# Kernel tuning notes

Measured on AMD Instinct MI355X. Metric: run time of the kernel, lower is better.

The kernel has to match this reference:

```python
import jax, jax.numpy as jnp
import numpy as np

# ---- static config (mirrors VectorQuantizer2.__init__) ----
V_PATCH = [1, 2, 3, 4, 6, 9, 13, 18, 24, 32]
SN = len(V_PATCH)
BETA = 0.25
QRESI = 0.5                      # Phi.resi_ratio = |quant_resi|
K_PHI = 4                        # share_quant_resi (PhiPartiallyShared)
TICKS = np.linspace(1.0 / 3 / K_PHI, 1.0 - 1.0 / 3 / K_PHI, K_PHI)  # K==4 branch
_A = -0.75                       # torch bicubic kernel coefficient


def _cubic(x):
    x = np.abs(x)
    return np.where(x <= 1.0, ((_A + 2.0) * x - (_A + 3.0)) * x * x + 1.0,
           np.where(x < 2.0, _A * (((x - 5.0) * x + 8.0) * x - 4.0), 0.0))


def _resize_mat(n_in, n_out, align_corners):
    # [n_out, n_in] separable torch-bicubic interpolation matrix (border-replicated)
    M = np.zeros((n_out, n_in), np.float32)
    for o in range(n_out):
        if align_corners:
            src = 0.0 if n_out == 1 else o * (n_in - 1) / (n_out - 1)
        else:
            src = (o + 0.5) * n_in / n_out - 0.5
        fl = int(np.floor(src)); t = src - fl
        for k in range(-1, 3):
            M[o, min(max(fl + k, 0), n_in - 1)] += float(_cubic(k - t))
    return jnp.asarray(M)


def _resize(x, hw, align_corners):
    # x: [B,C,H,W] -> [B,C,hw[0],hw[1]], bicubic, separable matmuls
    Mh = _resize_mat(x.shape[2], hw[0], align_corners)
    Mw = _resize_mat(x.shape[3], hw[1], align_corners)
    return jnp.einsum('oh,pw,bchw->bcop', Mh, Mw, x)


def _phi(h, w, b, r):
    # Phi: h*(1-r) + Conv3x3(h)*r
    y = jax.lax.conv_general_dilated(h, w, (1, 1), 'SAME',
                                     dimension_numbers=('NCHW', 'OIHW', 'NCHW'))
    y = y + b[None, :, None, None]
    return h * (1.0 - r) + y * r


def setup_inputs() -> dict:
    key = jax.random.key(0)
    k1, k2, k3 = jax.random.split(key, 3)
    B, C, H, W, V = 1024, 64, 32, 1, 4096
    f = jax.random.normal(k1, (B, C, H, W), jnp.float32)
    emb_weight = jax.random.normal(k2, (V, C), jnp.float32) * 0.02
    phi_w = jax.random.normal(k3, (K_PHI, C, C, 3, 3), jnp.float32) / np.sqrt(C * 9.0)
    phi_b = jnp.zeros((K_PHI, C), jnp.float32)
    return {"f_BChw": f, "emb_weight": emb_weight, "phi_w": phi_w, "phi_b": phi_b}


def reference(f_BChw, emb_weight, phi_w, phi_b):
    f = f_BChw.astype(jnp.float32)
    B, C, H, W = f.shape
    f_ng = jax.lax.stop_gradient(f)
    f_rest = f_ng
    f_hat = jnp.zeros_like(f_ng)
    e_ng = jax.lax.stop_gradient(emb_weight)
    e_sq = jnp.sum(e_ng * e_ng, axis=1)          # [V]
    loss = jnp.float32(0.0)
    levels = []
    for si, pn in enumerate(V_PATCH):
        ph, pw = pn, 1
        if si != SN - 1:
            rest = _resize(f_rest, (ph, pw), align_corners=True)
        else:
            rest = f                                  # last scale quantizes f itself
        rest_NC = jax.lax.stop_gradient(rest.transpose(0, 2, 3, 1).reshape(-1, C))
        d = jnp.sum(rest_NC * rest_NC, axis=1, keepdims=True) + e_sq \
            - 2.0 * (rest_NC @ e_ng.T)                # [N, V] squared distances
        idx = jnp.argmin(d, axis=1)                   # [N]
        h = emb_weight[idx.reshape(B, ph, pw)].transpose(0, 3, 1, 2)  # [B,C,ph,pw]
        if si != SN - 1:
            h = _resize(h, (H, W), align_corners=False)
        pi = int(np.argmin(np.abs(TICKS - si / (SN - 1))))
        h = _phi(h, phi_w[pi], phi_b[pi], QRESI)
        f_hat = f_hat + h
        f_rest = f_rest - h
        loss = loss + BETA * jnp.mean((jax.lax.stop_gradient(f_hat) - f) ** 2) \
                    + jnp.mean((f_hat - f_ng) ** 2)
        levels.append(f_hat)
    loss = loss / SN
    f_hat_st = jax.lax.stop_gradient(f_hat) - f_ng + f   # straight-through
    return f_hat_st, loss, jnp.stack(levels)
```

## Files before the change

kernel.cpp:

```cpp
#include <hip/hip_runtime.h>
#include <math.h>

#define BB 1024
#define CC 64
#define HH 32
#define VV 4096
#define NEL (BB*CC*HH)

#define RT 128

typedef __attribute__((ext_vector_type(4))) float f32x4;
typedef __attribute__((ext_vector_type(8))) short bf16x8;


__device__ double dev_cubic(double x){
#pragma clang fp contract(off)
  const double A = -0.75;
  x = fabs(x);
  if (x <= 1.0) return ((A + 2.0)*x - (A + 3.0))*x*x + 1.0;
  if (x < 2.0)  return A*(((x - 5.0)*x + 8.0)*x - 4.0);
  return 0.0;
}

__device__ __constant__ int c_vpatch[10] = {1,2,3,4,6,9,13,18,24,32};
__device__ __constant__ int c_pref[10]   = {0,1,3,6,10,16,25,38,56,80};

__global__ void gen_setup(float* Mdown, float* Mup, double* partial){
#pragma clang fp contract(off)
  int t = threadIdx.x;
  for (int i = t; i < 3584; i += 64) { Mdown[i] = 0.0f; Mup[i] = 0.0f; }
  if (t < 16) partial[t] = 0.0;
  __syncthreads();
  if (t < 20) {
    int si = t >> 1; int up = t & 1;
    int pn = c_vpatch[si];
    if (!up) {
      float* M = Mdown + c_pref[si]*32;
      for (int o = 0; o < pn; o++){
        double src = (pn == 1) ? 0.0 : (double)(o*(32-1)) / (double)(pn-1);
        double fl = floor(src); double tt = src - fl; int fli = (int)fl;
        for (int k = -1; k <= 2; k++){
          int j = fli + k; j = j < 0 ? 0 : (j > 31 ? 31 : j);
          float w = (float)dev_cubic((double)k - tt);
          M[o*32 + j] = M[o*32 + j] + w;
        }
      }
    } else {
      float* M = Mup + c_pref[si]*32;
      for (int o = 0; o < 32; o++){
        double src = ((double)o + 0.5) * (double)pn / 32.0 - 0.5;
        double fl = floor(src); double tt = src - fl; int fli = (int)fl;
        for (int k = -1; k <= 2; k++){
          int j = fli + k; j = j < 0 ? 0 : (j > pn-1 ? pn-1 : j);
          float w = (float)dev_cubic((double)k - tt);
          M[o*pn + j] = M[o*pn + j] + w;
        }
      }
    }
  }
}

__global__ void pack_w(const float* __restrict__ w, float* __restrict__ wPack){
  for (int e = blockIdx.x*blockDim.x + threadIdx.x; e < 4*64*196; e += gridDim.x*blockDim.x){
    int pi = e / (64*196);
    int r  = e - pi*64*196;
    int co = r / 196, m = r - co*196;
    float v = 0.0f;
    if (m < 192){
      int ci = m / 3, kh = m - ci*3;
      v = w[(((pi*64 + co)*64 + ci)*3 + kh)*3 + 1];
    }
    wPack[e] = v;
  }
}

__device__ float np_pairwise8_sq64(const float* a){
#pragma clang fp contract(off)
  float r0 = a[0]*a[0], r1 = a[1]*a[1], r2 = a[2]*a[2], r3 = a[3]*a[3];
  float r4 = a[4]*a[4], r5 = a[5]*a[5], r6 = a[6]*a[6], r7 = a[7]*a[7];
  for (int i = 8; i < 64; i += 8){
    float s0 = a[i+0]*a[i+0]; r0 = r0 + s0;
    float s1 = a[i+1]*a[i+1]; r1 = r1 + s1;
    float s2 = a[i+2]*a[i+2]; r2 = r2 + s2;
    float s3 = a[i+3]*a[i+3]; r3 = r3 + s3;
    float s4 = a[i+4]*a[i+4]; r4 = r4 + s4;
    float s5 = a[i+5]*a[i+5]; r5 = r5 + s5;
    float s6 = a[i+6]*a[i+6]; r6 = r6 + s6;
    float s7 = a[i+7]*a[i+7]; r7 = r7 + s7;
  }
  return ((r0 + r1) + (r2 + r3)) + ((r4 + r5) + (r6 + r7));
}

__device__ inline void split3t(float a, unsigned short& s1, unsigned short& s2, unsigned short& s3){
  unsigned u1 = __float_as_uint(a);
  s1 = (unsigned short)(u1 >> 16);
  float f1 = __uint_as_float(u1 & 0xffff0000u);
  float r1 = a - f1;
  unsigned u2 = __float_as_uint(r1);
  s2 = (unsigned short)(u2 >> 16);
  float f2 = __uint_as_float(u2 & 0xffff0000u);
  float r2 = r1 - f2;
  s3 = (unsigned short)(__float_as_uint(r2) >> 16);
}
__device__ inline float bf_up(short h){
  return __uint_as_float(((unsigned)(unsigned short)h) << 16);
}

__global__ void prep_emb(const float* __restrict__ emb, unsigned short* __restrict__ ePack,
                         float* __restrict__ e_sq){
#pragma clang fp contract(off)
  int v = blockIdx.x*blockDim.x + threadIdx.x;
  if (v >= VV) return;
  float row[64];
  for (int c = 0; c < CC; c++) row[c] = emb[v*CC + c];
  e_sq[v] = np_pairwise8_sq64(row);
  int vt = v >> 4, col = v & 15;
  for (int c = 0; c < CC; c++){
    unsigned short s1, s2, s3;
    split3t(row[c], s1, s2, s3);
    int kk = c >> 5, g = (c >> 3) & 3, jj = c & 7;
    size_t base = ((size_t)((vt*2 + kk)*3))*512 + (size_t)(g*16 + col)*8 + jj;
    ePack[base       ] = s1;
    ePack[base +  512] = s2;
    ePack[base + 1024] = s3;
  }
}

__global__ __launch_bounds__(256) void init_k(const float* __restrict__ f,
    float* frest, float* fhat, float* rest0, const float* Md0){
#pragma clang fp contract(off)
  __shared__ float frL[64][33];
  __shared__ float m0[32];
  int b = blockIdx.x, t = threadIdx.x;
  if (t < 32) m0[t] = Md0[t];
  for (int e = t; e < 2048; e += 256){
    int c = e >> 5, h = e & 31;
    float v = f[b*2048 + e];
    frL[c][h] = v;
    frest[b*2048 + e] = v;
    fhat[b*2048 + e] = 0.0f;
  }
  __syncthreads();
  if (t < 64){
    float s = 0.0f;
    for (int h = 0; h < 32; h++){ float pr = m0[h]*frL[t][h]; s = s + pr; }
    rest0[b*64 + t] = s;
  }
}


template<int PN, int NSPLIT>
__global__ __launch_bounds__(256,2) void argmin_mfma(const float* __restrict__ rest,
    const unsigned short* __restrict__ ePack, const float* __restrict__ e_sq,
    float* __restrict__ bestW, int* __restrict__ idxW)
{
#pragma clang fp contract(off)
  constexpr int VSPL = VV / NSPLIT;
  constexpr int NVT  = VSPL / 16;
  constexpr int CH   = 2;
  constexpr int NR   = NVT / CH;
  static_assert(NVT % CH == 0, "NVT must be multiple of CH");

  __shared__ __align__(16) unsigned short eS[2][CH*6*512];
  __shared__ float esL[VSPL];
  __shared__ float sR[RT];

  const int n0    = blockIdx.x * RT;
  const int split = blockIdx.y;
  const int v0    = split * VSPL;
  const int t     = threadIdx.x;
  const int lane  = t & 63;
  const int w     = t >> 6;
  const int m     = lane & 15;
  const int g     = lane >> 4;

  const unsigned short* gW = ePack + (size_t)(v0 >> 4)*3072
                           + (size_t)w*3*512 + (size_t)lane*8;
  bf16x8 st[3];
#pragma unroll
  for (int c = 0; c < 3; c++) st[c] = *(const bf16x8*)(gW + c*512);

  for (int e = t; e < VSPL; e += 256) esL[e] = e_sq[v0 + e];

  bf16x8 aF[2][2][3];
  const int rt0 = w*2;
#pragma unroll
  for (int r2 = 0; r2 < 2; r2++){
    int n = n0 + (rt0 + r2)*16 + m;
    int b = n / PN, p = n % PN;
    const float* rb = rest + (size_t)b*CC*PN + p;
#pragma unroll
    for (int kk = 0; kk < 2; kk++){
#pragma unroll
      for (int jj = 0; jj < 8; jj++){
        int c = kk*32 + g*8 + jj;
        float a = rb[(size_t)c*PN];
        unsigned short s1, s2, s3;
        split3t(a, s1, s2, s3);
        aF[r2][kk][0][jj] = (short)s1;
        aF[r2][kk][1][jj] = (short)s2;
        aF[r2][kk][2][jj] = (short)s3;
      }
    }
  }

  if (t < RT){
    int n = n0 + t;
    int b = n / PN, p = n % PN;
    const float* rb = rest + (size_t)b*CC*PN + p;
    float a0 = rb[0];              float r0 = a0*a0;
    float a1 = rb[(size_t)1*PN];   float r1 = a1*a1;
    float a2 = rb[(size_t)2*PN];   float r2 = a2*a2;
    float a3 = rb[(size_t)3*PN];   float r3 = a3*a3;
    float a4 = rb[(size_t)4*PN];   float r4 = a4*a4;
    float a5 = rb[(size_t)5*PN];   float r5 = a5*a5;
    float a6 = rb[(size_t)6*PN];   float r6 = a6*a6;
    float a7 = rb[(size_t)7*PN];   float r7 = a7*a7;
    for (int i = 8; i < 64; i += 8){
      float b0 = rb[(size_t)(i+0)*PN]; float s0 = b0*b0; r0 = r0 + s0;
      float b1 = rb[(size_t)(i+1)*PN]; float s1 = b1*b1; r1 = r1 + s1;
      float b2 = rb[(size_t)(i+2)*PN]; float s2 = b2*b2; r2 = r2 + s2;
      float b3 = rb[(size_t)(i+3)*PN]; float s3 = b3*b3; r3 = r3 + s3;
      float b4 = rb[(size_t)(i+4)*PN]; float s4 = b4*b4; r4 = r4 + s4;
      float b5 = rb[(size_t)(i+5)*PN]; float s5 = b5*b5; r5 = r5 + s5;
      float b6 = rb[(size_t)(i+6)*PN]; float s6 = b6*b6; r6 = r6 + s6;
      float b7 = rb[(size_t)(i+7)*PN]; float s7 = b7*b7; r7 = r7 + s7;
    }
    sR[t] = ((r0 + r1) + (r2 + r3)) + ((r4 + r5) + (r6 + r7));
  }

#pragma unroll
  for (int c = 0; c < 3; c++)
    *(bf16x8*)&eS[0][(w*3 + c)*512 + (size_t)lane*8] = st[c];
  __syncthreads();

  f32x4 sRl[2];
  sRl[0] = *(const f32x4*)&sR[(rt0+0)*16 + g*4];
  sRl[1] = *(const f32x4*)&sR[(rt0+1)*16 + g*4];

  float best[2][4]; int bidx[2][4];
#pragma unroll
  for (int r2 = 0; r2 < 2; r2++)
#pragma unroll
    for (int rg = 0; rg < 4; rg++){ best[r2][rg] = 3.0e38f; bidx[r2][rg] = 0; }

#define CTILE(eF, VT) do { \
    f32x4 acc0 = {0.f,0.f,0.f,0.f}; \
    f32x4 acc1 = {0.f,0.f,0.f,0.f}; \
    __builtin_amdgcn_s_setprio(1); \
    acc0 = __builtin_amdgcn_mfma_f32_16x16x32_bf16(aF[0][0][0], eF[0], acc0, 0,0,0); \
    acc1 = __builtin_amdgcn_mfma_f32_16x16x32_bf16(aF[1][0][0], eF[0], acc1, 0,0,0); \
    acc0 = __builtin_amdgcn_mfma_f32_16x16x32_bf16(aF[0][0][0], eF[1], acc0, 0,0,0); \
    acc1 = __builtin_amdgcn_mfma_f32_16x16x32_bf16(aF[1][0][0], eF[1], acc1, 0,0,0); \
    acc0 = __builtin_amdgcn_mfma_f32_16x16x32_bf16(aF[0][0][1], eF[0], acc0, 0,0,0); \
    acc1 = __builtin_amdgcn_mfma_f32_16x16x32_bf16(aF[1][0][1], eF[0], acc1, 0,0,0); \
    acc0 = __builtin_amdgcn_mfma_f32_16x16x32_bf16(aF[0][0][1], eF[1], acc0, 0,0,0); \
    acc1 = __builtin_amdgcn_mfma_f32_16x16x32_bf16(aF[1][0][1], eF[1], acc1, 0,0,0); \
    acc0 = __builtin_amdgcn_mfma_f32_16x16x32_bf16(aF[0][0][0], eF[2], acc0, 0,0,0); \
    acc1 = __builtin_amdgcn_mfma_f32_16x16x32_bf16(aF[1][0][0], eF[2], acc1, 0,0,0); \
    acc0 = __builtin_amdgcn_mfma_f32_16x16x32_bf16(aF[0][0][2], eF[0], acc0, 0,0,0); \
    acc1 = __builtin_amdgcn_mfma_f32_16x16x32_bf16(aF[1][0][2], eF[0], acc1, 0,0,0); \
    acc0 = __builtin_amdgcn_mfma_f32_16x16x32_bf16(aF[0][1][0], eF[3], acc0, 0,0,0); \
    acc1 = __builtin_amdgcn_mfma_f32_16x16x32_bf16(aF[1][1][0], eF[3], acc1, 0,0,0); \
    acc0 = __builtin_amdgcn_mfma_f32_16x16x32_bf16(aF[0][1][0], eF[4], acc0, 0,0,0); \
    acc1 = __builtin_amdgcn_mfma_f32_16x16x32_bf16(aF[1][1][0], eF[4], acc1, 0,0,0); \
    acc0 = __builtin_amdgcn_mfma_f32_16x16x32_bf16(aF[0][1][1], eF[3], acc0, 0,0,0); \
    acc1 = __builtin_amdgcn_mfma_f32_16x16x32_bf16(aF[1][1][1], eF[3], acc1, 0,0,0); \
    acc0 = __builtin_amdgcn_mfma_f32_16x16x32_bf16(aF[0][1][1], eF[4], acc0, 0,0,0); \
    acc1 = __builtin_amdgcn_mfma_f32_16x16x32_bf16(aF[1][1][1], eF[4], acc1, 0,0,0); \
    acc0 = __builtin_amdgcn_mfma_f32_16x16x32_bf16(aF[0][1][0], eF[5], acc0, 0,0,0); \
    acc1 = __builtin_amdgcn_mfma_f32_16x16x32_bf16(aF[1][1][0], eF[5], acc1, 0,0,0); \
    acc0 = __builtin_amdgcn_mfma_f32_16x16x32_bf16(aF[0][1][2], eF[3], acc0, 0,0,0); \
    acc1 = __builtin_amdgcn_mfma_f32_16x16x32_bf16(aF[1][1][2], eF[3], acc1, 0,0,0); \
    __builtin_amdgcn_s_setprio(0); \
    int vt_ = (VT); \
    float es = esL[vt_*16 + m]; \
    int codeBase = v0 + vt_*16 + m; \
    _Pragma("unroll") \
    for (int rg = 0; rg < 4; rg++){ \
      float t1a = sRl[0][rg] + es;                  \
      float da  = fmaf(-2.0f, acc0[rg], t1a);       \
      if (da < best[0][rg]) { best[0][rg] = da; bidx[0][rg] = codeBase; } \
      float t1b = sRl[1][rg] + es; \
      float db  = fmaf(-2.0f, acc1[rg], t1b); \
      if (db < best[1][rg]) { best[1][rg] = db; bidx[1][rg] = codeBase; } \
    } } while(0)

  int cur = 0;
  for (int r = 0; r < NR; r++){
    if (r + 1 < NR){
      const unsigned short* gR = gW + (size_t)(r+1)*CH*6*512;
#pragma unroll
      for (int c = 0; c < 3; c++) st[c] = *(const bf16x8*)(gR + c*512);
    }
#pragma unroll
    for (int q = 0; q < CH; q++){
      bf16x8 eF[6];
#pragma unroll
      for (int k = 0; k < 6; k++)
        eF[k] = *(const bf16x8*)&eS[cur][(q*6 + k)*512 + (size_t)lane*8];
      CTILE(eF, r*CH + q);
    }
    if (r + 1 < NR){
#pragma unroll
      for (int c = 0; c < 3; c++)
        *(bf16x8*)&eS[cur ^ 1][(w*3 + c)*512 + (size_t)lane*8] = st[c];
    }
    __syncthreads();
    cur ^= 1;
  }
#undef CTILE

#pragma unroll
  for (int r2 = 0; r2 < 2; r2++)
#pragma unroll
    for (int rg = 0; rg < 4; rg++){
      float v = best[r2][rg]; int ix = bidx[r2][rg];
      for (int off = 8; off; off >>= 1){
        float ov = __shfl_down(v, off, 16);
        int   oi = __shfl_down(ix, off, 16);
        if (ov < v || (ov == v && oi < ix)) { v = ov; ix = oi; }
      }
      if ((lane & 15) == 0){
        int n = n0 + (rt0 + r2)*16 + (lane>>4)*4 + rg;
        bestW[n*NSPLIT + split] = v;
        idxW [n*NSPLIT + split] = ix;
      }
    }
}


template<int PN, int PN2, int NSPLIT, bool LAST>
__global__ __launch_bounds__(256) void fused_phi(
    const float* __restrict__ emb,
    const float* __restrict__ bestW, const int* __restrict__ idxW,
    const float* __restrict__ Mup, const float* __restrict__ wP,
    const float* __restrict__ bias, const float* __restrict__ f,
    float* fhat, float* frest, float* levels_out, float* final_out,
    float* rest_next, const float* __restrict__ Mdown_next,
    double* partial, int si)
{
#pragma clang fp contract(off)
  __shared__ float huP[64][36];
  __shared__ union { float hE[24*64]; float frL[64*33]; } u;
  __shared__ float wL[64*196];
  __shared__ float mUp[32*25];
  __shared__ float mDn[32*33];
  __shared__ int idxL[32];
  __shared__ double red[4];
  int b = blockIdx.x, t = threadIdx.x;

  if (t < PN){
    int base = (b*PN + t)*NSPLIT;
    float v = bestW[base]; int ix = idxW[base];
#pragma unroll
    for (int s = 1; s < NSPLIT; s++){
      float ov = bestW[base + s];
      if (ov < v) { v = ov; ix = idxW[base + s]; }
    }
    idxL[t] = ix;
  }
  if (t < 64){ huP[t][0] = 0.0f; huP[t][33] = 0.0f; huP[t][34] = 0.0f; huP[t][35] = 0.0f; }
  for (int e = t; e < 3136; e += 256)
    *(float4*)&wL[e*4] = *(const float4*)&wP[e*4];
  if (PN2 > 0){
    for (int e = t; e < PN2*32; e += 256){
      int p = e >> 5, h = e & 31;
      mDn[p*33 + h] = Mdown_next[e];
    }
  }
  if (!LAST){
    for (int e = t; e < 32*PN; e += 256){
      int o = e / PN, p = e - o*PN;
      mUp[o*(PN+1) + p] = Mup[e];
    }
  }
  __syncthreads();

  if (!LAST){
    for (int e = t; e < PN*64; e += 256){
      int p = e >> 6, c = e & 63;
      u.hE[p*64 + c] = emb[idxL[p]*64 + c];
    }
    __syncthreads();
    for (int e = t; e < 2048; e += 256){
      int c = e >> 5, o = e & 31;
      const float* mr = &mUp[o*(PN+1)];
      float s = 0.0f;
#pragma unroll
      for (int p = 0; p < PN; p++){ float pr = mr[p]*u.hE[p*64 + c]; s = s + pr; }
      huP[c][1 + o] = s;
    }
  } else {
    for (int e = t; e < 2048; e += 256){
      int h = e >> 6, c = e & 63;
      huP[c][1 + h] = emb[idxL[h]*64 + c];
    }
  }
  __syncthreads();

  int co = t >> 2, h0 = (t & 3) * 8;
  float y[8];
#pragma unroll
  for (int uu = 0; uu < 8; uu++) y[uu] = 0.0f;
  for (int ci4 = 0; ci4 < 64; ci4 += 4){
    float4 wa = *(const float4*)&wL[co*196 + ci4*3];
    float4 wb = *(const float4*)&wL[co*196 + ci4*3 + 4];
    float4 wc = *(const float4*)&wL[co*196 + ci4*3 + 8];
    float wv[12] = {wa.x,wa.y,wa.z,wa.w, wb.x,wb.y,wb.z,wb.w, wc.x,wc.y,wc.z,wc.w};
#pragma unroll
    for (int q = 0; q < 4; q++){
      int ci = ci4 + q;
      float4 xa = *(const float4*)&huP[ci][h0];
      float4 xb = *(const float4*)&huP[ci][h0 + 4];
      float2 xc = *(const float2*)&huP[ci][h0 + 8];
      float x[10] = {xa.x,xa.y,xa.z,xa.w, xb.x,xb.y,xb.z,xb.w, xc.x,xc.y};
      float w0 = wv[q*3], w1 = wv[q*3+1], w2 = wv[q*3+2];
#pragma unroll
      for (int uu = 0; uu < 8; uu++){
        y[uu] = fmaf(w0, x[uu],   y[uu]);
        y[uu] = fmaf(w1, x[uu+1], y[uu]);
        y[uu] = fmaf(w2, x[uu+2], y[uu]);
      }
    }
  }

  float bb = bias[co];
  double lsum = 0.0;
  int base = b*2048 + co*32 + h0;
#pragma unroll
  for (int uu = 0; uu < 8; uu++){
    float yv = y[uu] + bb;
    float hp = 0.5f*huP[co][1 + h0 + uu] + 0.5f*yv;
    float fh = fhat[base+uu] + hp;
    fhat[base+uu] = fh;
    float fr = frest[base+uu] - hp;
    frest[base+uu] = fr;
    u.frL[co*33 + h0 + uu] = fr;
    float fv = f[base+uu];
    float dv = fh - fv;
    lsum += (double)dv*(double)dv;
    levels_out[base+uu] = fh;
    if (LAST) final_out[base+uu] = dv + fv;
  }
  for (int off = 32; off; off >>= 1) lsum += __shfl_down(lsum, off);
  if ((t & 63) == 0) red[t >> 6] = lsum;
  __syncthreads();

  if (PN2 > 0){
    for (int e = t; e < 64*PN2; e += 256){
      int c = e / PN2, p = e - c*PN2;
      const float* mr = &mDn[p*33];
      float s = 0.0f;
#pragma unroll
      for (int h = 0; h < 32; h++){ float pr = mr[h]*u.frL[c*33 + h]; s = s + pr; }
      rest_next[(b*64 + c)*PN2 + p] = s;
    }
  }
  if (t == 0) atomicAdd(&partial[si], red[0] + red[1] + red[2] + red[3]);
}

__global__ void finalize(const double* partial, float* out_loss){
#pragma clang fp contract(off)
  float L = 0.0f;
  for (int si = 0; si < 10; si++){
    float m = (float)(partial[si] / (double)NEL);
    float t1 = 0.25f * m;
    L = L + t1;
    L = L + m;
  }
  L = L / 10.0f;
  *out_loss = L;
}


struct Ptrs {
  const float *f, *emb;
  unsigned short *ePack;
  float *e_sq, *frest, *fhat, *rest, *Mdown, *Mup, *wPack, *bestW;
  int *idxW;
  double *partial;
  float *out0, *out_levels;
  const float *phi_b;
};

template<int PN, int PN2, int NSPLIT, bool LAST>
static void run_scale(const Ptrs& P, int si, int pi, int mup_off, int mdn_off,
                      hipStream_t stream){
  constexpr int N = BB*PN;
  dim3 ag(N/RT, NSPLIT);
  const float* restp = LAST ? P.f : P.rest;
  argmin_mfma<PN, NSPLIT><<<ag, 256, 0, stream>>>(restp, P.ePack, P.e_sq, P.bestW, P.idxW);
  fused_phi<PN, PN2, NSPLIT, LAST><<<BB, 256, 0, stream>>>(
      P.emb, P.bestW, P.idxW, P.Mup + mup_off,
      P.wPack + (size_t)pi*64*196, P.phi_b + (size_t)pi*CC,
      P.f, P.fhat, P.frest, P.out_levels + (size_t)si*NEL, P.out0,
      P.rest, P.Mdown + mdn_off, P.partial, si);
}

extern "C" void kernel_launch(void* const* d_in, const int* in_sizes, int n_in,
                              void* d_out, int out_size, void* d_ws, size_t ws_size,
                              hipStream_t stream) {
  const float* f     = (const float*)d_in[0];
  const float* emb   = (const float*)d_in[1];
  const float* phi_w = (const float*)d_in[2];
  const float* phi_b = (const float*)d_in[3];
  float* out0       = (float*)d_out;
  float* out_loss   = out0 + NEL;
  float* out_levels = out0 + NEL + 1;

  double* partial      = (double*)d_ws;
  unsigned short* ePack = (unsigned short*)(partial + 16);
  float*  e_sq    = (float*)(ePack + 786432 + 4096);
  float*  frest   = e_sq + 4096;
  float*  fhat    = frest + NEL;
  float*  rest    = fhat + NEL;
  float*  Mdown   = rest + NEL;
  float*  Mup     = Mdown + 3584;
  float*  wPack   = Mup + 3584;
  float*  bestW   = wPack + 50176;
  int*    idxW    = (int*)(bestW + 262144);

  double q = 1.0/3.0; q = q/4.0;
  double start = q;
  double stop  = 1.0 - q;
  double delta = stop - start;
  double step  = delta/3.0;
  double ticks[4];
  ticks[0] = start;
  ticks[1] = step + start;
  { double t2 = 2.0*step; ticks[2] = t2 + start; }
  ticks[3] = stop;
  int pi_tab[10];
  for (int si = 0; si < 10; si++){
    double x = (double)si / 9.0;
    int bi = 0; double bd = fabs(ticks[0] - x);
    for (int i2 = 1; i2 < 4; i2++){
      double dd = fabs(ticks[i2] - x);
      if (dd < bd) { bd = dd; bi = i2; }
    }
    pi_tab[si] = bi;
  }

  static const int pref[10] = {0,1,3,6,10,16,25,38,56,80};

  gen_setup<<<1, 64, 0, stream>>>(Mdown, Mup, partial);
  pack_w<<<64, 256, 0, stream>>>(phi_w, wPack);
  prep_emb<<<16, 256, 0, stream>>>(emb, ePack, e_sq);
  init_k<<<BB, 256, 0, stream>>>(f, frest, fhat, rest, Mdown );

  Ptrs P = {f, emb, ePack, e_sq, frest, fhat, rest, Mdown, Mup, wPack, bestW,
            idxW, partial, out0, out_levels, phi_b};

  run_scale< 1,  2, 32, false>(P, 0, pi_tab[0], pref[0]*32, pref[1]*32, stream);
  run_scale< 2,  3, 32, false>(P, 1, pi_tab[1], pref[1]*32, pref[2]*32, stream);
  run_scale< 3,  4, 32, false>(P, 2, pi_tab[2], pref[2]*32, pref[3]*32, stream);
  run_scale< 4,  6, 32, false>(P, 3, pi_tab[3], pref[3]*32, pref[4]*32, stream);
  run_scale< 6,  9, 16, false>(P, 4, pi_tab[4], pref[4]*32, pref[5]*32, stream);
  run_scale< 9, 13, 16, false>(P, 5, pi_tab[5], pref[5]*32, pref[6]*32, stream);
  run_scale<13, 18,  8, false>(P, 6, pi_tab[6], pref[6]*32, pref[7]*32, stream);
  run_scale<18, 24,  8, false>(P, 7, pi_tab[7], pref[7]*32, pref[8]*32, stream);
  run_scale<24,  0,  8, false>(P, 8, pi_tab[8], pref[8]*32, 0,          stream);
  run_scale<32,  0,  8, true >(P, 9, pi_tab[9], pref[9]*32, 0,          stream);

  finalize<<<1, 1, 0, stream>>>(partial, out_loss);
}
```

Measured before the change: 1.010 ms.

## Merge setup kernels into one launch and read conv weights from global

Folds the four setup kernels (interp matrices, weight packing, embedding split/pack, state init) into one kernel whose blocks pick a role by blockIdx. This removes launch gaps and runs the setup jobs side by side. The first downsample is now computed as a direct copy of f[h=0] instead of a weighted sum, relying on the align_corners scale-1 matrix being [1,0,...]. The embedding pack now uses a shared-memory staging pass with vectorized stores. fused_phi no longer stages the 50KB weight tile in LDS and reads it from global/cache instead, which cuts LDS use and may raise occupancy, at the risk of slower weight loads.

```diff
diff --git a/kernel.cpp b/kernel.cpp
--- a/kernel.cpp
+++ b/kernel.cpp
@@ -24,55 +24,6 @@
 
 __device__ __constant__ int c_vpatch[10] = {1,2,3,4,6,9,13,18,24,32};
 __device__ __constant__ int c_pref[10]   = {0,1,3,6,10,16,25,38,56,80};
-
-__global__ void gen_setup(float* Mdown, float* Mup, double* partial){
-#pragma clang fp contract(off)
-  int t = threadIdx.x;
-  for (int i = t; i < 3584; i += 64) { Mdown[i] = 0.0f; Mup[i] = 0.0f; }
-  if (t < 16) partial[t] = 0.0;
-  __syncthreads();
-  if (t < 20) {
-    int si = t >> 1; int up = t & 1;
-    int pn = c_vpatch[si];
-    if (!up) {
-      float* M = Mdown + c_pref[si]*32;
-      for (int o = 0; o < pn; o++){
-        double src = (pn == 1) ? 0.0 : (double)(o*(32-1)) / (double)(pn-1);
-        double fl = floor(src); double tt = src - fl; int fli = (int)fl;
-        for (int k = -1; k <= 2; k++){
-          int j = fli + k; j = j < 0 ? 0 : (j > 31 ? 31 : j);
-          float w = (float)dev_cubic((double)k - tt);
-          M[o*32 + j] = M[o*32 + j] + w;
-        }
-      }
-    } else {
-      float* M = Mup + c_pref[si]*32;
-      for (int o = 0; o < 32; o++){
-        double src = ((double)o + 0.5) * (double)pn / 32.0 - 0.5;
-        double fl = floor(src); double tt = src - fl; int fli = (int)fl;
-        for (int k = -1; k <= 2; k++){
-          int j = fli + k; j = j < 0 ? 0 : (j > pn-1 ? pn-1 : j);
-          float w = (float)dev_cubic((double)k - tt);
-          M[o*pn + j] = M[o*pn + j] + w;
-        }
-      }
-    }
-  }
-}
-
-__global__ void pack_w(const float* __restrict__ w, float* __restrict__ wPack){
-  for (int e = blockIdx.x*blockDim.x + threadIdx.x; e < 4*64*196; e += gridDim.x*blockDim.x){
-    int pi = e / (64*196);
-    int r  = e - pi*64*196;
-    int co = r / 196, m = r - co*196;
-    float v = 0.0f;
-    if (m < 192){
-      int ci = m / 3, kh = m - ci*3;
-      v = w[(((pi*64 + co)*64 + ci)*3 + kh)*3 + 1];
-    }
-    wPack[e] = v;
-  }
-}
 
 __device__ float np_pairwise8_sq64(const float* a){
 #pragma clang fp contract(off)
@@ -102,49 +53,98 @@
   float r2 = r1 - f2;
   s3 = (unsigned short)(__float_as_uint(r2) >> 16);
 }
-__device__ inline float bf_up(short h){
-  return __uint_as_float(((unsigned)(unsigned short)h) << 16);
-}
-
-__global__ void prep_emb(const float* __restrict__ emb, unsigned short* __restrict__ ePack,
-                         float* __restrict__ e_sq){
+
+__global__ __launch_bounds__(256) void setup_all(
+    const float* __restrict__ f, const float* __restrict__ emb,
+    const float* __restrict__ phi_w,
+    float* frest, float* fhat, float* rest0,
+    float* Mdown, float* Mup, double* partial,
+    float* wPack, unsigned short* ePack, float* e_sq)
+{
 #pragma clang fp contract(off)
-  int v = blockIdx.x*blockDim.x + threadIdx.x;
-  if (v >= VV) return;
-  float row[64];
-  for (int c = 0; c < CC; c++) row[c] = emb[v*CC + c];
-  e_sq[v] = np_pairwise8_sq64(row);
-  int vt = v >> 4, col = v & 15;
-  for (int c = 0; c < CC; c++){
-    unsigned short s1, s2, s3;
-    split3t(row[c], s1, s2, s3);
-    int kk = c >> 5, g = (c >> 3) & 3, jj = c & 7;
-    size_t base = ((size_t)((vt*2 + kk)*3))*512 + (size_t)(g*16 + col)*8 + jj;
-    ePack[base       ] = s1;
-    ePack[base +  512] = s2;
-    ePack[base + 1024] = s3;
-  }
-}
-
-__global__ __launch_bounds__(256) void init_k(const float* __restrict__ f,
-    float* frest, float* fhat, float* rest0, const float* Md0){
-#pragma clang fp contract(off)
-  __shared__ float frL[64][33];
-  __shared__ float m0[32];
-  int b = blockIdx.x, t = threadIdx.x;
-  if (t < 32) m0[t] = Md0[t];
-  for (int e = t; e < 2048; e += 256){
-    int c = e >> 5, h = e & 31;
-    float v = f[b*2048 + e];
-    frL[c][h] = v;
-    frest[b*2048 + e] = v;
-    fhat[b*2048 + e] = 0.0f;
-  }
-  __syncthreads();
-  if (t < 64){
-    float s = 0.0f;
-    for (int h = 0; h < 32; h++){ float pr = m0[h]*frL[t][h]; s = s + pr; }
-    rest0[b*64 + t] = s;
+  __shared__ float rows[64][65];
+  int blk = blockIdx.x, t = threadIdx.x;
+
+  if (blk < 1024){
+    int b = blk;
+    for (int e = t; e < 2048; e += 256){
+      float v = f[b*2048 + e];
+      frest[b*2048 + e] = v;
+      fhat[b*2048 + e] = 0.0f;
+    }
+    if (t < 64) rest0[b*64 + t] = f[b*2048 + t*32];
+  } else if (blk < 1088){
+    int e0 = (blk - 1024)*784;
+    for (int i = t; i < 784; i += 256){
+      int e = e0 + i;
+      int pi = e / (64*196);
+      int r  = e - pi*64*196;
+      int co = r / 196, m = r - co*196;
+      float v = 0.0f;
+      if (m < 192){
+        int ci = m / 3, kh = m - ci*3;
+        v = phi_w[(((pi*64 + co)*64 + ci)*3 + kh)*3 + 1];
+      }
+      wPack[e] = v;
+    }
+  } else if (blk < 1152){
+    int v0 = (blk - 1088)*64;
+    for (int e = t; e < 4096; e += 256){
+      int vl = e >> 6, c = e & 63;
+      rows[vl][c] = emb[(size_t)(v0 + vl)*64 + c];
+    }
+    __syncthreads();
+    if (t < 64){
+      int v = v0 + t;
+      e_sq[v] = np_pairwise8_sq64(&rows[t][0]);
+      int vt = v >> 4, col = v & 15;
+#pragma unroll
+      for (int o = 0; o < 8; o++){
+        bf16x8 v1, v2, v3;
+#pragma unroll
+        for (int jj = 0; jj < 8; jj++){
+          unsigned short s1, s2, s3;
+          split3t(rows[t][o*8 + jj], s1, s2, s3);
+          v1[jj] = (short)s1; v2[jj] = (short)s2; v3[jj] = (short)s3;
+        }
+        int kk = o >> 2, g = o & 3;
+        size_t base = ((size_t)((vt*2 + kk)*3))*512 + (size_t)(g*16 + col)*8;
+        *(bf16x8*)&ePack[base       ] = v1;
+        *(bf16x8*)&ePack[base +  512] = v2;
+        *(bf16x8*)&ePack[base + 1024] = v3;
+      }
+    }
+  } else {
+    for (int i = t; i < 3584; i += 256) { Mdown[i] = 0.0f; Mup[i] = 0.0f; }
+    if (t < 16) partial[t] = 0.0;
+    __syncthreads();
+    if (t < 20) {
+      int si = t >> 1; int up = t & 1;
+      int pn = c_vpatch[si];
+      if (!up) {
+        float* M = Mdown + c_pref[si]*32;
+        for (int o = 0; o < pn; o++){
+          double src = (pn == 1) ? 0.0 : (double)(o*(32-1)) / (double)(pn-1);
+          double fl = floor(src); double tt = src - fl; int fli = (int)fl;
+          for (int k = -1; k <= 2; k++){
+            int j = fli + k; j = j < 0 ? 0 : (j > 31 ? 31 : j);
+            float w = (float)dev_cubic((double)k - tt);
+            M[o*32 + j] = M[o*32 + j] + w;
+          }
+        }
+      } else {
+        float* M = Mup + c_pref[si]*32;
+        for (int o = 0; o < 32; o++){
+          double src = ((double)o + 0.5) * (double)pn / 32.0 - 0.5;
+          double fl = floor(src); double tt = src - fl; int fli = (int)fl;
+          for (int k = -1; k <= 2; k++){
+            int j = fli + k; j = j < 0 ? 0 : (j > pn-1 ? pn-1 : j);
+            float w = (float)dev_cubic((double)k - tt);
+            M[o*pn + j] = M[o*pn + j] + w;
+          }
+        }
+      }
+    }
   }
 }
 
@@ -343,7 +343,6 @@
 #pragma clang fp contract(off)
   __shared__ float huP[64][36];
   __shared__ union { float hE[24*64]; float frL[64*33]; } u;
-  __shared__ float wL[64*196];
   __shared__ float mUp[32*25];
   __shared__ float mDn[32*33];
   __shared__ int idxL[32];
@@ -361,8 +360,6 @@
     idxL[t] = ix;
   }
   if (t < 64){ huP[t][0] = 0.0f; huP[t][33] = 0.0f; huP[t][34] = 0.0f; huP[t][35] = 0.0f; }
-  for (int e = t; e < 3136; e += 256)
-    *(float4*)&wL[e*4] = *(const float4*)&wP[e*4];
   if (PN2 > 0){
     for (int e = t; e < PN2*32; e += 256){
       int p = e >> 5, h = e & 31;
@@ -404,9 +401,9 @@
 #pragma unroll
   for (int uu = 0; uu < 8; uu++) y[uu] = 0.0f;
   for (int ci4 = 0; ci4 < 64; ci4 += 4){
-    float4 wa = *(const float4*)&wL[co*196 + ci4*3];
-    float4 wb = *(const float4*)&wL[co*196 + ci4*3 + 4];
-    float4 wc = *(const float4*)&wL[co*196 + ci4*3 + 8];
+    float4 wa = *(const float4*)&wP[co*196 + ci4*3];
+    float4 wb = *(const float4*)&wP[co*196 + ci4*3 + 4];
+    float4 wc = *(const float4*)&wP[co*196 + ci4*3 + 8];
     float wv[12] = {wa.x,wa.y,wa.z,wa.w, wb.x,wb.y,wb.z,wb.w, wc.x,wc.y,wc.z,wc.w};
 #pragma unroll
     for (int q = 0; q < 4; q++){
@@ -511,7 +508,7 @@
 
   double* partial      = (double*)d_ws;
   unsigned short* ePack = (unsigned short*)(partial + 16);
-  float*  e_sq    = (float*)(ePack + 786432 + 4096);
+  float*  e_sq    = (float*)(ePack + 786432 + 16384);
   float*  frest   = e_sq + 4096;
   float*  fhat    = frest + NEL;
   float*  rest    = fhat + NEL;
@@ -544,10 +541,8 @@
 
   static const int pref[10] = {0,1,3,6,10,16,25,38,56,80};
 
-  gen_setup<<<1, 64, 0, stream>>>(Mdown, Mup, partial);
-  pack_w<<<64, 256, 0, stream>>>(phi_w, wPack);
-  prep_emb<<<16, 256, 0, stream>>>(emb, ePack, e_sq);
-  init_k<<<BB, 256, 0, stream>>>(f, frest, fhat, rest, Mdown );
+  setup_all<<<1153, 256, 0, stream>>>(f, emb, phi_w, frest, fhat, rest,
+                                      Mdown, Mup, partial, wPack, ePack, e_sq);
 
   Ptrs P = {f, emb, ePack, e_sq, frest, fhat, rest, Mdown, Mup, wPack, bestW,
             idxW, partial, out0, out_levels, phi_b};
```

Result: no change. 1.012 ms (+0.3%).
